# Kernel optimization log

Hardware: AMD Instinct MI355X
Metric: run time of the kernel (lower is better)

## Reference

```python
import jax, jax.numpy as jnp
import numpy as np

B = 256; NROIS = 200; IN = 200; HID = 128; L = 4; H = 8; RATIO = 0.5
K = int(np.ceil(RATIO * NROIS))        # SAGPooling top-k per graph = 100
N = B * NROIS                          # total nodes = 51200
DEG = 32; EPG = NROIS * DEG; E_EDGES = B * EPG  # 1,638,400 edges
EMB = HID * L                          # MHA embed dim = 512
DH = EMB // H

def _xavier(k, shape):
    fan_in, fan_out = shape[-2], shape[-1]
    lim = float(np.sqrt(6.0 / (fan_in + fan_out)))
    return jax.random.uniform(k, shape, jnp.float32, -lim, lim)

def setup_inputs() -> dict:
    key = jax.random.key(0)
    ks = jax.random.split(key, 16)
    x = jax.random.normal(ks[0], (N, IN), jnp.float32)
    # block-diagonal edge list: edges stay within each graph's node range
    src = jax.random.randint(ks[1], (E_EDGES,), 0, NROIS, jnp.int32)
    dst = jax.random.randint(ks[2], (E_EDGES,), 0, NROIS, jnp.int32)
    off = jnp.repeat(jnp.arange(B, dtype=jnp.int32) * NROIS, EPG)
    edge_index = jnp.stack([src + off, dst + off])
    edge_attr = jax.random.normal(ks[3], (E_EDGES,), jnp.float32)  # unused by the math
    batch = jnp.repeat(jnp.arange(B, dtype=jnp.int32), NROIS)
    return dict(
        x=x, edge_index=edge_index, edge_attr=edge_attr, batch=batch,
        gcn_w0=_xavier(ks[4], (IN, HID)),
        gcn_w=_xavier(ks[5], (L - 1, HID, HID)),
        gcn_b=jnp.zeros((L, HID), jnp.float32),
        lin1_w0=_xavier(ks[6], (IN + HID, HID)),
        lin1_w=_xavier(ks[7], (L - 1, 2 * HID, HID)),
        lin1_b=jnp.zeros((L, HID), jnp.float32),
        lin2_w=_xavier(ks[8], (L, HID, HID)),
        lin2_b=jnp.zeros((L, HID), jnp.float32),
        sag_w1=_xavier(ks[9], (HID, 1)),
        sag_w2=_xavier(ks[10], (HID, 1)),
        sag_b=jnp.zeros((1,), jnp.float32),
        mha_in_w=_xavier(ks[11], (3 * EMB, EMB)),
        mha_in_b=jnp.zeros((3 * EMB,), jnp.float32),
        mha_out_w=_xavier(ks[12], (EMB, EMB)),
        mha_out_b=jnp.zeros((EMB,), jnp.float32),
        fin_w=_xavier(ks[13], (EMB, HID)),
        fin_b=jnp.zeros((HID,), jnp.float32),
    )

def _gcn_conv(x, src, dst, W, b):
    xw = x @ W
    deg = jax.ops.segment_sum(jnp.ones_like(dst, jnp.float32), dst, num_segments=N) + 1.0
    dinv = jax.lax.rsqrt(deg)
    norm = dinv[src] * dinv[dst]                     # [E]
    agg = jax.ops.segment_sum(xw[src] * norm[:, None], dst, num_segments=N)
    agg = agg + xw * (dinv * dinv)[:, None]          # self-loop term
    return agg + b

def _gcblock(x, src, dst, gw, gb, l1w, l1b, l2w, l2b):
    x1 = jnp.tanh(_gcn_conv(x, src, dst, gw, gb))
    h = jnp.tanh(jnp.concatenate([x, x1], axis=1) @ l1w + l1b)
    return jnp.tanh(h @ l2w + l2b)

def _sag_pool_pad(z, src, dst, w1, w2, b):
    # SAGPooling score via PyG GraphConv (aggr='add'): lin_rel(sum_j x_j) + lin_root(x_i)
    neigh = jax.ops.segment_sum(z[src], dst, num_segments=N)
    score = (neigh @ w1)[:, 0] + b[0] + (z @ w2)[:, 0]        # [N]
    s3 = score.reshape(B, NROIS)
    vals, idx = jax.lax.top_k(s3, K)                           # [B,K]
    z3 = z.reshape(B, NROIS, HID)
    pooled = jnp.take_along_axis(z3, idx[:, :, None], axis=1) * jnp.tanh(vals)[:, :, None]
    zpad = jnp.zeros_like(z3).at[jnp.arange(B)[:, None], idx].set(pooled)
    return zpad.reshape(N, HID)

def reference(x, edge_index, edge_attr, batch,
              gcn_w0, gcn_w, gcn_b, lin1_w0, lin1_w, lin1_b, lin2_w, lin2_b,
              sag_w1, sag_w2, sag_b,
              mha_in_w, mha_in_b, mha_out_w, mha_out_b, fin_w, fin_b):
    src, dst = edge_index[0], edge_index[1]
    z = x
    pads = []
    for i in range(L):
        gw = gcn_w0 if i == 0 else gcn_w[i - 1]
        l1w = lin1_w0 if i == 0 else lin1_w[i - 1]
        z = _gcblock(z, src, dst, gw, gcn_b[i], l1w, lin1_b[i], lin2_w[i], lin2_b[i])
        pads.append(_sag_pool_pad(z, src, dst, sag_w1, sag_w2, sag_b))
    xc = jnp.concatenate(pads, axis=1).reshape(B, NROIS, EMB)   # [B,S,E]
    # MultiheadAttention (batch_first, eval mode -> no dropout)
    qkv = xc @ mha_in_w.T + mha_in_b                             # [B,S,3E]
    q, k, v = jnp.split(qkv, 3, axis=-1)
    def heads(t):
        return t.reshape(B, NROIS, H, DH).transpose(0, 2, 1, 3)  # [B,H,S,dh]
    q, k, v = heads(q), heads(k), heads(v)
    scores = jnp.einsum('bhqd,bhkd->bhqk', q, k) / np.sqrt(DH)
    attn = jax.nn.softmax(scores, axis=-1)                       # [B,H,S,S]
    o = jnp.einsum('bhqk,bhkd->bhqd', attn, v).transpose(0, 2, 1, 3).reshape(B, NROIS, EMB)
    o = o @ mha_out_w.T + mha_out_b
    attn_weights = attn.mean(axis=1)                             # avg over heads [B,S,S]
    # readout: global_mean_pool over each graph's nrois nodes
    pooled = o.mean(axis=1)                                      # [B,E]
    out = jnp.tanh(pooled @ fin_w + fin_b)                       # [B,HID]
    return out, attn_weights
```

## Files before the change

kernel.cpp:

```cpp
#include <hip/hip_runtime.h>
#include <hip/hip_fp16.h>


#define GB   256
#define SS   200
#define KIN  200
#define HD   128
#define NLAY 4
#define NHD  8
#define TOPK 100
#define NT   (GB * SS)
#define EPG_ 6400
#define NE_  (GB * EPG_)
#define EMB_ 512

typedef _Float16 half8 __attribute__((ext_vector_type(8)));
typedef _Float16 half4v __attribute__((ext_vector_type(4)));
typedef float floatx4 __attribute__((ext_vector_type(4)));

__global__ __launch_bounds__(256) void k_build_A(const int* __restrict__ src,
                                                 const int* __restrict__ dst,
                                                 float* __restrict__ A) {
  int e = blockIdx.x * 256 + threadIdx.x;
  if (e >= NE_) return;
  int d = dst[e], s = src[e];
  int b = d / SS;
  int dl = d - b * SS;
  int sl = s - b * SS;
  atomicAdd(&A[((size_t)b * SS + dl) * SS + sl], 1.0f);
}

__global__ __launch_bounds__(256) void k_dinv(const float* __restrict__ A,
                                              float* __restrict__ dinv) {
  int node = blockIdx.x * 4 + (threadIdx.x >> 6);
  int lane = threadIdx.x & 63;
  const float* r = A + (size_t)node * SS;
  float v = r[lane] + r[lane + 64] + r[lane + 128];
  if (lane < 8) v += r[lane + 192];
#pragma unroll
  for (int o = 32; o; o >>= 1) v += __shfl_xor(v, o);
  if (lane == 0) dinv[node] = rsqrtf(v + 1.0f);
}

__global__ __launch_bounds__(256) void k_prep_all(
    const float* __restrict__ gcn_w0, const float* __restrict__ gcn_w,
    const float* __restrict__ lin1_w0, const float* __restrict__ lin1_w,
    const float* __restrict__ lin2_w,
    __half* __restrict__ whi, __half* __restrict__ wlo) {
  const int mat = blockIdx.x >> 7;
  const int n   = blockIdx.x & 127;
  const int l = mat / 3, which = mat % 3;
  const float* src;
  int K, Kpad;
  if (which == 0) {
    K = l ? HD : KIN;  Kpad = l ? 128 : 256;
    src = l ? gcn_w + (size_t)(l - 1) * HD * HD : gcn_w0;
  } else if (which == 1) {
    K = l ? 2 * HD : KIN + HD;  Kpad = l ? 256 : 384;
    src = l ? lin1_w + (size_t)(l - 1) * 2 * HD * HD : lin1_w0;
  } else {
    K = HD;  Kpad = HD;
    src = lin2_w + (size_t)l * HD * HD;
  }
  int off = (l == 0) ? (which == 0 ? 0 : (which == 1 ? 32768 : 81920))
                     : 98304 + (l - 1) * 65536 +
                       (which == 0 ? 0 : (which == 1 ? 16384 : 49152));
  _Float16* wh = (_Float16*)whi + (size_t)off + (size_t)n * Kpad;
  _Float16* wl = (_Float16*)wlo + (size_t)off + (size_t)n * Kpad;
  for (int k = threadIdx.x; k < Kpad; k += 256) {
    float v = (k < K) ? src[(size_t)k * HD + n] : 0.f;
    _Float16 h = (_Float16)v;
    wh[k] = h;
    wl[k] = (_Float16)(v - (float)h);
  }
}

__global__ __launch_bounds__(256) void k_prep_w16(const float* __restrict__ W,
                                                  __half* __restrict__ W16) {
  int i = blockIdx.x * 256 + threadIdx.x;
  float4 v = reinterpret_cast<const float4*>(W)[i];
  half4v h = {(_Float16)v.x, (_Float16)v.y, (_Float16)v.z, (_Float16)v.w};
  *reinterpret_cast<half4v*>((_Float16*)W16 + (size_t)i * 4) = h;
}

__global__ __launch_bounds__(256) void k_node_mfma(
    const float* __restrict__ in1, int k1,
    const float* __restrict__ in2,
    const __half* __restrict__ Whi, const __half* __restrict__ Wlo,
    int Kpad,
    const float* __restrict__ bias,
    float* __restrict__ out, int doTanh) {
  const int m0 = blockIdx.x * 64;
  const int t = threadIdx.x;
  const int wave = t >> 6, lane = t & 63;
  const int col = lane & 15, quad = lane >> 4;
  const int wm = (wave & 1) * 32;
  const int wn = (wave >> 1) * 64;
  __shared__ __align__(16) _Float16 Ah[64][72];
  __shared__ __align__(16) _Float16 Al[64][72];
  floatx4 acc[2][4] = {};
  const int lr = t >> 2;
  const int lk = (t & 3) * 16;
  const _Float16* Wh = (const _Float16*)Whi;
  const _Float16* Wl = (const _Float16*)Wlo;

  for (int k0 = 0; k0 < Kpad; k0 += 64) {
    __syncthreads();
#pragma unroll
    for (int q = 0; q < 4; ++q) {
      int kg = k0 + lk + q * 4;
      float4 v = {0.f, 0.f, 0.f, 0.f};
      if (kg < k1)
        v = *reinterpret_cast<const float4*>(&in1[(size_t)(m0 + lr) * k1 + kg]);
      else if (in2 && kg < k1 + HD)
        v = *reinterpret_cast<const float4*>(&in2[(size_t)(m0 + lr) * HD + (kg - k1)]);
      half4v h = {(_Float16)v.x, (_Float16)v.y, (_Float16)v.z, (_Float16)v.w};
      half4v lo = {(_Float16)(v.x - (float)h.x), (_Float16)(v.y - (float)h.y),
                   (_Float16)(v.z - (float)h.z), (_Float16)(v.w - (float)h.w)};
      *reinterpret_cast<half4v*>(&Ah[lr][lk + q * 4]) = h;
      *reinterpret_cast<half4v*>(&Al[lr][lk + q * 4]) = lo;
    }
    __syncthreads();
#pragma unroll
    for (int ks = 0; ks < 2; ++ks) {
      half8 ah[2], al[2], bh[4], bl[4];
#pragma unroll
      for (int i = 0; i < 2; ++i) {
        ah[i] = *reinterpret_cast<const half8*>(&Ah[wm + i * 16 + col][ks * 32 + quad * 8]);
        al[i] = *reinterpret_cast<const half8*>(&Al[wm + i * 16 + col][ks * 32 + quad * 8]);
      }
#pragma unroll
      for (int j = 0; j < 4; ++j) {
        const size_t wo = (size_t)(wn + j * 16 + col) * Kpad + k0 + ks * 32 + quad * 8;
        bh[j] = *reinterpret_cast<const half8*>(Wh + wo);
        bl[j] = *reinterpret_cast<const half8*>(Wl + wo);
      }
#pragma unroll
      for (int i = 0; i < 2; ++i)
#pragma unroll
        for (int j = 0; j < 4; ++j) {
          acc[i][j] = __builtin_amdgcn_mfma_f32_16x16x32_f16(ah[i], bh[j], acc[i][j], 0, 0, 0);
          acc[i][j] = __builtin_amdgcn_mfma_f32_16x16x32_f16(ah[i], bl[j], acc[i][j], 0, 0, 0);
          acc[i][j] = __builtin_amdgcn_mfma_f32_16x16x32_f16(al[i], bh[j], acc[i][j], 0, 0, 0);
        }
    }
  }
#pragma unroll
  for (int j = 0; j < 4; ++j) {
    int n = wn + j * 16 + col;
    float bb = bias ? bias[n] : 0.f;
#pragma unroll
    for (int i = 0; i < 2; ++i) {
      int rbase = m0 + wm + i * 16 + quad * 4;
#pragma unroll
      for (int r = 0; r < 4; ++r) {
        float v = acc[i][j][r] + bb;
        if (doTanh) v = tanhf(v);
        out[(size_t)(rbase + r) * HD + n] = v;
      }
    }
  }
}

__global__ __launch_bounds__(256) void k_fused(
    const float* __restrict__ in1, int k1,
    const float* __restrict__ x1,
    const __half* __restrict__ l1wh, const __half* __restrict__ l1wl, int KP1,
    const float* __restrict__ l1b,
    const __half* __restrict__ l2wh, const __half* __restrict__ l2wl,
    const float* __restrict__ l2b,
    const __half* __restrict__ gwh, const __half* __restrict__ gwl,
    float* __restrict__ zout, float* __restrict__ xwout) {
  const int m0 = blockIdx.x * 64;
  const int t = threadIdx.x;
  const int wave = t >> 6, lane = t & 63;
  const int col = lane & 15, quad = lane >> 4;
  const int wm = (wave & 1) * 32;
  const int wn = (wave >> 1) * 64;
  __shared__ __align__(16) _Float16 Ah[64][72];
  __shared__ __align__(16) _Float16 Al[64][72];
  __shared__ __align__(16) _Float16 Hh[64][136];
  __shared__ __align__(16) _Float16 Hl[64][136];
  const int lr = t >> 2;
  const int lk = (t & 3) * 16;

  {
    floatx4 acc[2][4] = {};
    for (int k0 = 0; k0 < KP1; k0 += 64) {
      __syncthreads();
#pragma unroll
      for (int q = 0; q < 4; ++q) {
        int kg = k0 + lk + q * 4;
        float4 v = {0.f, 0.f, 0.f, 0.f};
        if (kg < k1)
          v = *reinterpret_cast<const float4*>(&in1[(size_t)(m0 + lr) * k1 + kg]);
        else if (kg < k1 + HD)
          v = *reinterpret_cast<const float4*>(&x1[(size_t)(m0 + lr) * HD + (kg - k1)]);
        half4v h = {(_Float16)v.x, (_Float16)v.y, (_Float16)v.z, (_Float16)v.w};
        half4v lo = {(_Float16)(v.x - (float)h.x), (_Float16)(v.y - (float)h.y),
                     (_Float16)(v.z - (float)h.z), (_Float16)(v.w - (float)h.w)};
        *reinterpret_cast<half4v*>(&Ah[lr][lk + q * 4]) = h;
        *reinterpret_cast<half4v*>(&Al[lr][lk + q * 4]) = lo;
      }
      __syncthreads();
#pragma unroll
      for (int ks = 0; ks < 2; ++ks) {
        half8 ah[2], al[2], bh[4], bl[4];
#pragma unroll
        for (int i = 0; i < 2; ++i) {
          ah[i] = *reinterpret_cast<const half8*>(&Ah[wm + i * 16 + col][ks * 32 + quad * 8]);
          al[i] = *reinterpret_cast<const half8*>(&Al[wm + i * 16 + col][ks * 32 + quad * 8]);
        }
#pragma unroll
        for (int j = 0; j < 4; ++j) {
          const size_t wo = (size_t)(wn + j * 16 + col) * KP1 + k0 + ks * 32 + quad * 8;
          bh[j] = *reinterpret_cast<const half8*>((const _Float16*)l1wh + wo);
          bl[j] = *reinterpret_cast<const half8*>((const _Float16*)l1wl + wo);
        }
#pragma unroll
        for (int i = 0; i < 2; ++i)
#pragma unroll
          for (int j = 0; j < 4; ++j) {
            acc[i][j] = __builtin_amdgcn_mfma_f32_16x16x32_f16(ah[i], bh[j], acc[i][j], 0, 0, 0);
            acc[i][j] = __builtin_amdgcn_mfma_f32_16x16x32_f16(ah[i], bl[j], acc[i][j], 0, 0, 0);
            acc[i][j] = __builtin_amdgcn_mfma_f32_16x16x32_f16(al[i], bh[j], acc[i][j], 0, 0, 0);
          }
      }
    }
#pragma unroll
    for (int j = 0; j < 4; ++j) {
      int n = wn + j * 16 + col;
      float bb = l1b[n];
#pragma unroll
      for (int i = 0; i < 2; ++i) {
        int rb = wm + i * 16 + quad * 4;
#pragma unroll
        for (int r = 0; r < 4; ++r) {
          float v = tanhf(acc[i][j][r] + bb);
          _Float16 h = (_Float16)v;
          Hh[rb + r][n] = h;
          Hl[rb + r][n] = (_Float16)(v - (float)h);
        }
      }
    }
  }
  __syncthreads();

  {
    floatx4 acc[2][4] = {};
#pragma unroll
    for (int kc = 0; kc < 4; ++kc) {
      half8 ah[2], al[2], bh[4], bl[4];
#pragma unroll
      for (int i = 0; i < 2; ++i) {
        ah[i] = *reinterpret_cast<const half8*>(&Hh[wm + i * 16 + col][kc * 32 + quad * 8]);
        al[i] = *reinterpret_cast<const half8*>(&Hl[wm + i * 16 + col][kc * 32 + quad * 8]);
      }
#pragma unroll
      for (int j = 0; j < 4; ++j) {
        const size_t wo = (size_t)(wn + j * 16 + col) * HD + kc * 32 + quad * 8;
        bh[j] = *reinterpret_cast<const half8*>((const _Float16*)l2wh + wo);
        bl[j] = *reinterpret_cast<const half8*>((const _Float16*)l2wl + wo);
      }
#pragma unroll
      for (int i = 0; i < 2; ++i)
#pragma unroll
        for (int j = 0; j < 4; ++j) {
          acc[i][j] = __builtin_amdgcn_mfma_f32_16x16x32_f16(ah[i], bh[j], acc[i][j], 0, 0, 0);
          acc[i][j] = __builtin_amdgcn_mfma_f32_16x16x32_f16(ah[i], bl[j], acc[i][j], 0, 0, 0);
          acc[i][j] = __builtin_amdgcn_mfma_f32_16x16x32_f16(al[i], bh[j], acc[i][j], 0, 0, 0);
        }
    }
    __syncthreads();
#pragma unroll
    for (int j = 0; j < 4; ++j) {
      int n = wn + j * 16 + col;
      float bb = l2b[n];
#pragma unroll
      for (int i = 0; i < 2; ++i) {
        int rb = wm + i * 16 + quad * 4;
#pragma unroll
        for (int r = 0; r < 4; ++r) {
          float v = tanhf(acc[i][j][r] + bb);
          zout[(size_t)(m0 + rb + r) * HD + n] = v;
          _Float16 h = (_Float16)v;
          Hh[rb + r][n] = h;
          Hl[rb + r][n] = (_Float16)(v - (float)h);
        }
      }
    }
  }
  if (!gwh) return;
  __syncthreads();

  {
    floatx4 acc[2][4] = {};
#pragma unroll
    for (int kc = 0; kc < 4; ++kc) {
      half8 ah[2], al[2], bh[4], bl[4];
#pragma unroll
      for (int i = 0; i < 2; ++i) {
        ah[i] = *reinterpret_cast<const half8*>(&Hh[wm + i * 16 + col][kc * 32 + quad * 8]);
        al[i] = *reinterpret_cast<const half8*>(&Hl[wm + i * 16 + col][kc * 32 + quad * 8]);
      }
#pragma unroll
      for (int j = 0; j < 4; ++j) {
        const size_t wo = (size_t)(wn + j * 16 + col) * HD + kc * 32 + quad * 8;
        bh[j] = *reinterpret_cast<const half8*>((const _Float16*)gwh + wo);
        bl[j] = *reinterpret_cast<const half8*>((const _Float16*)gwl + wo);
      }
#pragma unroll
      for (int i = 0; i < 2; ++i)
#pragma unroll
        for (int j = 0; j < 4; ++j) {
          acc[i][j] = __builtin_amdgcn_mfma_f32_16x16x32_f16(ah[i], bh[j], acc[i][j], 0, 0, 0);
          acc[i][j] = __builtin_amdgcn_mfma_f32_16x16x32_f16(ah[i], bl[j], acc[i][j], 0, 0, 0);
          acc[i][j] = __builtin_amdgcn_mfma_f32_16x16x32_f16(al[i], bh[j], acc[i][j], 0, 0, 0);
        }
    }
#pragma unroll
    for (int j = 0; j < 4; ++j) {
      int n = wn + j * 16 + col;
#pragma unroll
      for (int i = 0; i < 2; ++i) {
        int rb = wm + i * 16 + quad * 4;
#pragma unroll
        for (int r = 0; r < 4; ++r)
          xwout[(size_t)(m0 + rb + r) * HD + n] = acc[i][j][r];
      }
    }
  }
}

__global__ __launch_bounds__(256) void k_agg_mfma(
    const float* __restrict__ A, const float* __restrict__ dinv,
    const float* __restrict__ xw, const float* __restrict__ bias,
    float* __restrict__ out) {
  const int b    = blockIdx.x >> 1;
  const int row0 = (blockIdx.x & 1) * 128;
  const int t = threadIdx.x;
  const int wave = t >> 6, lane = t & 63;
  const int col = lane & 15, quad = lane >> 4;
  const int wm = (wave & 1) * 64, wn = (wave >> 1) * 64;
  __shared__ __align__(16) _Float16 Ah[128][72];
  __shared__ __align__(16) _Float16 Bh[128][72];
  __shared__ __align__(16) _Float16 Bl[128][72];
  __shared__ float dvs[256];
  dvs[t] = (t < SS) ? dinv[b * SS + t] : 0.f;
  floatx4 acc[4][4] = {};
  const float* Ab  = A  + (size_t)b * SS * SS;
  const float* xwb = xw + (size_t)b * SS * HD;
  const int lr = t >> 1, lk = (t & 1) * 32;
  const int d = row0 + lr;
  __syncthreads();

  for (int k0 = 0; k0 < 256; k0 += 64) {
    __syncthreads();
#pragma unroll
    for (int q = 0; q < 8; ++q) {
      int s = k0 + lk + q * 4;
      float4 v = {0.f, 0.f, 0.f, 0.f};
      if (d < SS && s < SS)
        v = *reinterpret_cast<const float4*>(&Ab[(size_t)d * SS + s]);
      if (s + 0 == d) v.x += 1.0f;
      if (s + 1 == d) v.y += 1.0f;
      if (s + 2 == d) v.z += 1.0f;
      if (s + 3 == d) v.w += 1.0f;
      half4v h = {(_Float16)v.x, (_Float16)v.y, (_Float16)v.z, (_Float16)v.w};
      *reinterpret_cast<half4v*>(&Ah[lr][lk + q * 4]) = h;
    }
#pragma unroll
    for (int p = 0; p < 8; ++p) {
      int idx = t + p * 256;
      int c4 = idx & 31, ss = idx >> 5;
      int s = k0 + ss;
      float4 v = {0.f, 0.f, 0.f, 0.f};
      if (s < SS)
        v = *reinterpret_cast<const float4*>(&xwb[(size_t)s * HD + c4 * 4]);
      float dvv = dvs[s & 255];
      int ssx = ss ^ ((c4 & 7) << 3);
      float e[4] = {v.x * dvv, v.y * dvv, v.z * dvv, v.w * dvv};
#pragma unroll
      for (int j = 0; j < 4; ++j) {
        _Float16 h = (_Float16)e[j];
        Bh[c4 * 4 + j][ssx] = h;
        Bl[c4 * 4 + j][ssx] = (_Float16)(e[j] - (float)h);
      }
    }
    __syncthreads();
#pragma unroll
    for (int ks = 0; ks < 2; ++ks) {
      half8 ah[4], bh[4], bl[4];
#pragma unroll
      for (int i = 0; i < 4; ++i)
        ah[i] = *reinterpret_cast<const half8*>(&Ah[wm + i * 16 + col][ks * 32 + quad * 8]);
#pragma unroll
      for (int j = 0; j < 4; ++j) {
        int n = wn + j * 16 + col;
        int koff = (ks * 32 + quad * 8) ^ (((n >> 2) & 7) << 3);
        bh[j] = *reinterpret_cast<const half8*>(&Bh[n][koff]);
        bl[j] = *reinterpret_cast<const half8*>(&Bl[n][koff]);
      }
#pragma unroll
      for (int i = 0; i < 4; ++i)
#pragma unroll
        for (int j = 0; j < 4; ++j) {
          acc[i][j] = __builtin_amdgcn_mfma_f32_16x16x32_f16(ah[i], bh[j], acc[i][j], 0, 0, 0);
          acc[i][j] = __builtin_amdgcn_mfma_f32_16x16x32_f16(ah[i], bl[j], acc[i][j], 0, 0, 0);
        }
    }
  }
#pragma unroll
  for (int j = 0; j < 4; ++j) {
    int n = wn + j * 16 + col;
    float bb = bias[n];
#pragma unroll
    for (int i = 0; i < 4; ++i) {
      int rbase = row0 + wm + i * 16 + quad * 4;
#pragma unroll
      for (int r = 0; r < 4; ++r) {
        int row = rbase + r;
        if (row < SS)
          out[((size_t)b * SS + row) * HD + n] = tanhf(dvs[row] * acc[i][j][r] + bb);
      }
    }
  }
}

__global__ __launch_bounds__(256) void k_sag(
    const float* __restrict__ z, const float* __restrict__ A,
    const float* __restrict__ w1, const float* __restrict__ w2,
    const float* __restrict__ sb,
    __half* __restrict__ xch, __half* __restrict__ xcl, int layer) {
  const int b = blockIdx.x, t = threadIdx.x;
  __shared__ float w1s[HD], w2s[HD];
  __shared__ float zw1[SS], sc[SS], fac[SS];
  if (t < HD) { w1s[t] = w1[t]; w2s[t] = w2[t]; }
  __syncthreads();
  float a2 = 0.f;
  if (t < SS) {
    const float4* zr = reinterpret_cast<const float4*>(&z[((size_t)b * SS + t) * HD]);
    float a1 = 0.f;
#pragma unroll
    for (int q = 0; q < HD / 4; ++q) {
      float4 v = zr[q];
      a1 += v.x * w1s[4 * q] + v.y * w1s[4 * q + 1] + v.z * w1s[4 * q + 2] + v.w * w1s[4 * q + 3];
      a2 += v.x * w2s[4 * q] + v.y * w2s[4 * q + 1] + v.z * w2s[4 * q + 2] + v.w * w2s[4 * q + 3];
    }
    zw1[t] = a1;
  }
  __syncthreads();
  if (t < SS) {
    float s0 = 0.f, s1 = 0.f, s2 = 0.f, s3 = 0.f;
    const float4* ar = reinterpret_cast<const float4*>(&A[((size_t)b * SS + t) * SS]);
#pragma unroll
    for (int q = 0; q < SS / 4; q += 4) {
      float4 v0 = ar[q], v1 = ar[q + 1];
      float4 v2 = (q + 2 < SS / 4) ? ar[q + 2] : float4{0.f, 0.f, 0.f, 0.f};
      float4 v3 = (q + 3 < SS / 4) ? ar[q + 3] : float4{0.f, 0.f, 0.f, 0.f};
      s0 += v0.x * zw1[4 * q] + v0.y * zw1[4 * q + 1] + v0.z * zw1[4 * q + 2] + v0.w * zw1[4 * q + 3];
      s1 += v1.x * zw1[4 * q + 4] + v1.y * zw1[4 * q + 5] + v1.z * zw1[4 * q + 6] + v1.w * zw1[4 * q + 7];
      if (q + 2 < SS / 4)
        s2 += v2.x * zw1[4 * q + 8] + v2.y * zw1[4 * q + 9] + v2.z * zw1[4 * q + 10] + v2.w * zw1[4 * q + 11];
      if (q + 3 < SS / 4)
        s3 += v3.x * zw1[4 * q + 12] + v3.y * zw1[4 * q + 13] + v3.z * zw1[4 * q + 14] + v3.w * zw1[4 * q + 15];
    }
    sc[t] = sb[0] + a2 + ((s0 + s1) + (s2 + s3));
  }
  __syncthreads();
  if (t < SS) {
    float si = sc[t];
    int cnt = 0;
    for (int j = 0; j < SS; ++j) {
      float sj = sc[j];
      cnt += (sj > si || (sj == si && j < t)) ? 1 : 0;
    }
    fac[t] = (cnt < TOPK) ? tanhf(si) : 0.f;
  }
  __syncthreads();
  _Float16* xh = (_Float16*)xch;
  _Float16* xl = (_Float16*)xcl;
  for (int idx = t; idx < SS * HD; idx += 256) {
    int row = idx >> 7, c = idx & 127;
    float v = fac[row] * z[((size_t)b * SS + row) * HD + c];
    _Float16 h = (_Float16)v;
    size_t o = ((size_t)b * SS + row) * EMB_ + layer * HD + c;
    xh[o] = h;
    xl[o] = (_Float16)(v - (float)h);
  }
}

__global__ __launch_bounds__(256) void k_proj(
    const __half* __restrict__ xch, const __half* __restrict__ Win16,
    const float* __restrict__ bin, __half* __restrict__ QKh) {
  const int wg = (blockIdx.x & 7) * 400 + (blockIdx.x >> 3);
  const int bm = wg >> 3;
  const int bn = wg & 7;
  const int m0 = bm * 128, n0 = bn * 128;
  const int t = threadIdx.x;
  const int wave = t >> 6, lane = t & 63;
  const int col = lane & 15, quad = lane >> 4;
  const int wm = (wave & 1) * 64;
  const int wn = (wave >> 1) * 64;
  __shared__ __align__(16) _Float16 As[128][64];
  __shared__ __align__(16) _Float16 Bs[128][64];
  floatx4 acc[4][4] = {};
  const _Float16* X = (const _Float16*)xch;
  const _Float16* W = (const _Float16*)Win16;

  const int srow = lane >> 3;
  const int sch  = (lane & 7) ^ srow;
  const int arow = wave * 8 + srow;
  const int fsw = col & 7;

  for (int k0 = 0; k0 < EMB_; k0 += 64) {
#pragma unroll
    for (int q = 0; q < 4; ++q) {
      const _Float16* ga = X + (size_t)(m0 + q * 32 + arow) * EMB_ + k0 + sch * 8;
      __builtin_amdgcn_global_load_lds(
          (const __attribute__((address_space(1))) void*)ga,
          (__attribute__((address_space(3))) void*)((char*)&As[0][0] + q * 4096 + wave * 1024),
          16, 0, 0);
      const _Float16* gb = W + (size_t)(n0 + q * 32 + arow) * EMB_ + k0 + sch * 8;
      __builtin_amdgcn_global_load_lds(
          (const __attribute__((address_space(1))) void*)gb,
          (__attribute__((address_space(3))) void*)((char*)&Bs[0][0] + q * 4096 + wave * 1024),
          16, 0, 0);
    }
    __syncthreads();
#pragma unroll
    for (int ks = 0; ks < 2; ++ks) {
      const int ch = (ks * 4 + quad) ^ fsw;
      half8 af[4], bf[4];
#pragma unroll
      for (int i = 0; i < 4; ++i)
        af[i] = *reinterpret_cast<const half8*>(
            (const char*)&As[0][0] + (wm + i * 16 + col) * 128 + ch * 16);
#pragma unroll
      for (int j = 0; j < 4; ++j)
        bf[j] = *reinterpret_cast<const half8*>(
            (const char*)&Bs[0][0] + (wn + j * 16 + col) * 128 + ch * 16);
#pragma unroll
      for (int i = 0; i < 4; ++i)
#pragma unroll
        for (int j = 0; j < 4; ++j)
          acc[i][j] = __builtin_amdgcn_mfma_f32_16x16x32_f16(af[i], bf[j], acc[i][j], 0, 0, 0);
    }
    __syncthreads();
  }
#pragma unroll
  for (int j = 0; j < 4; ++j) {
    int c = n0 + wn + j * 16 + col;
    float bb = bin[c];
#pragma unroll
    for (int i = 0; i < 4; ++i) {
      int rbase = m0 + wm + i * 16 + quad * 4;
#pragma unroll
      for (int r = 0; r < 4; ++r)
        QKh[(size_t)(rbase + r) * 1024 + c] = __float2half(acc[i][j][r] + bb);
    }
  }
}

__global__ __launch_bounds__(256) void k_attn(
    const __half* __restrict__ QKh,
    float* __restrict__ cpbuf,
    float* __restrict__ attn) {
  const int bx = (blockIdx.x & 7) * 416 + (blockIdx.x >> 3);
  const int b  = bx / 13;
  const int it = bx % 13;
  const int i0 = it * 16;
  const int rows = (SS - i0 >= 16) ? 16 : (SS - i0);
  const int t    = threadIdx.x;
  const int wave = t >> 6;
  const int lane = t & 63;
  const int col  = lane & 15;
  const int quad = lane >> 4;
  const int srow_ = t >> 4;
  const int ssub_ = t & 15;

  __shared__ __align__(16) float Ss[16][212];

  float am[13];
  int   soff[13];
  int   kmax = 0;
#pragma unroll
  for (int k = 0; k < 13; ++k) {
    int idx = t + (k << 8);
    am[k] = 0.f;
    if (idx < rows * 200) {
      int i = idx / 200;
      soff[k] = idx + 12 * i;
      kmax = k + 1;
    } else soff[k] = 0;
  }

  const _Float16* Qbase = (const _Float16*)QKh + (size_t)b * SS * 1024;
  const _Float16* qrow = Qbase + (size_t)(i0 + col) * 1024 + quad * 8;
  const _Float16* krow[4];
#pragma unroll
  for (int m = 0; m < 4; ++m) {
    int jt = wave + m * 4;
    krow[m] = Qbase + (size_t)(jt * 16 + col) * 1024 + 512 + quad * 8;
  }

  for (int h = 0; h < NHD; ++h) {
    const int hoff = h * 64;
    half8 a0 = *reinterpret_cast<const half8*>(qrow + hoff);
    half8 a1 = *reinterpret_cast<const half8*>(qrow + hoff + 32);
#pragma unroll
    for (int m = 0; m < 4; ++m) {
      int jt = wave + m * 4;
      if (jt < 13) {
        half8 b0 = *reinterpret_cast<const half8*>(krow[m] + hoff);
        half8 b1 = *reinterpret_cast<const half8*>(krow[m] + hoff + 32);
        floatx4 acc = {0.f, 0.f, 0.f, 0.f};
        acc = __builtin_amdgcn_mfma_f32_16x16x32_f16(a0, b0, acc, 0, 0, 0);
        acc = __builtin_amdgcn_mfma_f32_16x16x32_f16(a1, b1, acc, 0, 0, 0);
#pragma unroll
        for (int r = 0; r < 4; ++r)
          Ss[quad * 4 + r][jt * 16 + col] = acc[r] * 0.125f;
      }
    }
    __syncthreads();
    if (srow_ < rows) {
      float v[13];
      float mx = -1e30f;
#pragma unroll
      for (int i2 = 0; i2 < 13; ++i2) {
        int c = ssub_ + i2 * 16;
        v[i2] = (c < 200) ? Ss[srow_][c] : -1e30f;
        mx = fmaxf(mx, v[i2]);
      }
#pragma unroll
      for (int m = 8; m; m >>= 1) mx = fmaxf(mx, __shfl_xor(mx, m));
      float sum = 0.f;
#pragma unroll
      for (int i2 = 0; i2 < 13; ++i2) {
        v[i2] = __expf(v[i2] - mx);
        sum += v[i2];
      }
#pragma unroll
      for (int m = 8; m; m >>= 1) sum += __shfl_xor(sum, m);
      float rl = 1.0f / sum;
#pragma unroll
      for (int i2 = 0; i2 < 13; ++i2) {
        int c = ssub_ + i2 * 16;
        if (c < 200) Ss[srow_][c] = v[i2] * rl;
      }
    }
    __syncthreads();
    const float* sflat = &Ss[0][0];
#pragma unroll
    for (int k = 0; k < 13; ++k)
      if (k < kmax) am[k] += sflat[soff[k]] * 0.125f;
    if (t < SS) {
      float s = 0.f;
      for (int i = 0; i < rows; ++i) s += Ss[i][t];
      atomicAdd(&cpbuf[((size_t)b * NHD + h) * SS + t], s);
    }
    __syncthreads();
  }
  float* abase = &attn[((size_t)b * SS + i0) * SS];
#pragma unroll
  for (int k = 0; k < 13; ++k)
    if (k < kmax) abase[t + (k << 8)] = am[k];
}

__global__ __launch_bounds__(256) void k_pool(
    const __half* __restrict__ xch, const __half* __restrict__ xcl,
    const float* __restrict__ cpbuf,
    const float* __restrict__ Win, const float* __restrict__ bin,
    float* __restrict__ pooled) {
  const int b = blockIdx.x, t = threadIdx.x;
  __shared__ float cps[NHD][SS];
  __shared__ float tvs[NHD][EMB_];
  for (int idx = t; idx < NHD * SS; idx += 256) {
    int h = idx / SS, j = idx - h * SS;
    cps[h][j] = cpbuf[((size_t)b * NHD + h) * SS + j];
  }
  __syncthreads();
  const _Float16* xh = (const _Float16*)xch + (size_t)b * SS * EMB_;
  const _Float16* xl = (const _Float16*)xcl + (size_t)b * SS * EMB_;
  float a0[NHD] = {0.f}, a1[NHD] = {0.f};
  for (int j = 0; j < SS; ++j) {
    float x0 = (float)xh[(size_t)j * EMB_ + t] + (float)xl[(size_t)j * EMB_ + t];
    float x1 = (float)xh[(size_t)j * EMB_ + t + 256] + (float)xl[(size_t)j * EMB_ + t + 256];
#pragma unroll
    for (int h = 0; h < NHD; ++h) {
      float c = cps[h][j];
      a0[h] += c * x0; a1[h] += c * x1;
    }
  }
#pragma unroll
  for (int h = 0; h < NHD; ++h) { tvs[h][t] = a0[h]; tvs[h][t + 256] = a1[h]; }
  __syncthreads();
  const int wv = t >> 6, lane = t & 63;
  for (int e = wv; e < EMB_; e += 4) {
    int h = e >> 6;
    const float* wr = Win + (size_t)(2 * EMB_ + e) * EMB_;
    float s = 0.f;
#pragma unroll
    for (int q = 0; q < 8; ++q) s += wr[lane + q * 64] * tvs[h][lane + q * 64];
#pragma unroll
    for (int o = 32; o; o >>= 1) s += __shfl_xor(s, o);
    if (lane == 0) pooled[(size_t)b * EMB_ + e] = bin[2 * EMB_ + e] * (float)SS + s;
  }
}

__global__ __launch_bounds__(256) void k_final(
    const float* __restrict__ pooled, const float* __restrict__ Wout,
    const float* __restrict__ bout, const float* __restrict__ finw,
    const float* __restrict__ finb, float* __restrict__ out) {
  const int b = blockIdx.x, t = threadIdx.x;
  __shared__ float pl[EMB_], po[EMB_];
  for (int k = t; k < EMB_; k += 256) pl[k] = pooled[(size_t)b * EMB_ + k] * (1.0f / (float)SS);
  __syncthreads();
  for (int e = t; e < EMB_; e += 256) {
    const float* wr = &Wout[(size_t)e * EMB_];
    float a = bout[e];
    for (int k = 0; k < EMB_; ++k) a += wr[k] * pl[k];
    po[e] = a;
  }
  __syncthreads();
  if (t < HD) {
    float a = finb[t];
    for (int e = 0; e < EMB_; ++e) a += po[e] * finw[(size_t)e * HD + t];
    out[(size_t)b * HD + t] = tanhf(a);
  }
}

extern "C" void kernel_launch(void* const* d_in, const int* in_sizes, int n_in,
                              void* d_out, int out_size, void* d_ws, size_t ws_size,
                              hipStream_t stream) {
  const float* x         = (const float*)d_in[0];
  const int*   ei        = (const int*)d_in[1];
  const float* gcn_w0    = (const float*)d_in[4];
  const float* gcn_w     = (const float*)d_in[5];
  const float* gcn_b     = (const float*)d_in[6];
  const float* lin1_w0   = (const float*)d_in[7];
  const float* lin1_w    = (const float*)d_in[8];
  const float* lin1_b    = (const float*)d_in[9];
  const float* lin2_w    = (const float*)d_in[10];
  const float* lin2_b    = (const float*)d_in[11];
  const float* sag_w1    = (const float*)d_in[12];
  const float* sag_w2    = (const float*)d_in[13];
  const float* sag_b     = (const float*)d_in[14];
  const float* mha_in_w  = (const float*)d_in[15];
  const float* mha_in_b  = (const float*)d_in[16];
  const float* mha_out_w = (const float*)d_in[17];
  const float* mha_out_b = (const float*)d_in[18];
  const float* fin_w     = (const float*)d_in[19];
  const float* fin_b     = (const float*)d_in[20];

  float* ws     = (float*)d_ws;
  float* dinv   = ws;
  float* Araw   = dinv + NT;
  float* buf0   = Araw + (size_t)GB * SS * SS;
  float* buf1   = buf0 + (size_t)NT * HD;
  float* zbuf   = buf1 + (size_t)NT * HD;
  float* xcf    = zbuf + (size_t)NT * HD;
  __half* xch   = (__half*)xcf;
  __half* xcl   = xch + (size_t)NT * EMB_;
  float* pooled = xcf + (size_t)NT * EMB_;
  __half* QKh  = (__half*)Araw;
  float* cpbuf = Araw + 26214400;

  float* outp = (float*)d_out;
  float* attn = outp + (size_t)GB * HD;

  __half* whi   = (__half*)attn;
  __half* wlo   = whi + 294912;
  __half* Win16 = wlo + 294912;

  hipMemsetAsync(Araw, 0, (size_t)GB * SS * SS * sizeof(float), stream);

  k_prep_all<<<12 * 128, 256, 0, stream>>>(gcn_w0, gcn_w, lin1_w0, lin1_w, lin2_w, whi, wlo);
  k_prep_w16<<<512, 256, 0, stream>>>(mha_in_w, Win16);
  k_build_A<<<NE_ / 256, 256, 0, stream>>>(ei, ei + NE_, Araw);
  k_dinv<<<NT / 4, 256, 0, stream>>>(Araw, dinv);

  static const int KP1[4]  = {384, 256, 256, 256};
  static const int OFFg[4] = {0, 98304, 163840, 229376};
  static const int OFF1[4] = {32768, 114688, 180224, 245760};
  static const int OFF2[4] = {81920, 147456, 212992, 278528};

  k_node_mfma<<<NT / 64, 256, 0, stream>>>(x, KIN, nullptr,
                                           whi + OFFg[0], wlo + OFFg[0], 256,
                                           nullptr, buf0, 0);

  for (int l = 0; l < NLAY; ++l) {
    const float* zin = (l == 0) ? x : zbuf;
    int k1 = (l == 0) ? KIN : HD;
    k_agg_mfma<<<GB * 2, 256, 0, stream>>>(Araw, dinv, buf0, gcn_b + l * HD, buf1);
    k_fused<<<NT / 64, 256, 0, stream>>>(
        zin, k1, buf1,
        whi + OFF1[l], wlo + OFF1[l], KP1[l], lin1_b + l * HD,
        whi + OFF2[l], wlo + OFF2[l], lin2_b + l * HD,
        (l < NLAY - 1) ? whi + OFFg[l + 1] : (const __half*)nullptr,
        (l < NLAY - 1) ? wlo + OFFg[l + 1] : (const __half*)nullptr,
        zbuf, buf0);
    k_sag<<<GB, 256, 0, stream>>>(zbuf, Araw, sag_w1, sag_w2, sag_b, xch, xcl, l);
  }

  hipMemsetAsync(cpbuf, 0, (size_t)GB * NHD * SS * sizeof(float), stream);
  k_proj<<<(NT / 128) * 8, 256, 0, stream>>>(xch, Win16, mha_in_b, QKh);
  k_attn<<<GB * 13, 256, 0, stream>>>(QKh, cpbuf, attn);
  k_pool<<<GB, 256, 0, stream>>>(xch, xcl, cpbuf, mha_in_w, mha_in_b, pooled);
  k_final<<<GB, 256, 0, stream>>>(pooled, mha_out_w, mha_out_b, fin_w, fin_b, outp);
}
```

Before: 1.411 ms.

## Convert adjacency to fp16 once and stream it into LDS via direct global loads

Adds a one-time pass that converts the dense per-graph adjacency matrix to fp16 (with padding). The aggregation kernel then loads A tiles straight into LDS with global_load_lds using an XOR swizzle, and moves the self-loop term into the epilogue as dinv^2 * xw. The SAG scoring kernel also reads the fp16 adjacency. This halves A traffic across the four layers and drops per-element conversion work, at the cost of an extra conversion kernel, extra workspace, and relying on edge counts being exactly representable in fp16.

```diff
diff --git a/kernel.cpp b/kernel.cpp
--- a/kernel.cpp
+++ b/kernel.cpp
@@ -13,6 +13,8 @@
 #define EPG_ 6400
 #define NE_  (GB * EPG_)
 #define EMB_ 512
+#define NA_  (GB * SS * SS)
+#define NA_PAD (NA_ + 16384)
 
 typedef _Float16 half8 __attribute__((ext_vector_type(8)));
 typedef _Float16 half4v __attribute__((ext_vector_type(4)));
@@ -40,6 +42,18 @@
 #pragma unroll
   for (int o = 32; o; o >>= 1) v += __shfl_xor(v, o);
   if (lane == 0) dinv[node] = rsqrtf(v + 1.0f);
+}
+
+__global__ __launch_bounds__(256) void k_prep_a16(const float* __restrict__ A,
+                                                  __half* __restrict__ A16) {
+  size_t i4 = ((size_t)blockIdx.x * 256 + threadIdx.x) * 4;
+  if (i4 >= NA_PAD) return;
+  half4v h = {(_Float16)0.f, (_Float16)0.f, (_Float16)0.f, (_Float16)0.f};
+  if (i4 < NA_) {
+    float4 v = *reinterpret_cast<const float4*>(A + i4);
+    h = {(_Float16)v.x, (_Float16)v.y, (_Float16)v.z, (_Float16)v.w};
+  }
+  *reinterpret_cast<half4v*>((_Float16*)A16 + i4) = h;
 }
 
 __global__ __launch_bounds__(256) void k_prep_all(
@@ -333,7 +347,7 @@
 }
 
 __global__ __launch_bounds__(256) void k_agg_mfma(
-    const float* __restrict__ A, const float* __restrict__ dinv,
+    const __half* __restrict__ A16, const float* __restrict__ dinv,
     const float* __restrict__ xw, const float* __restrict__ bias,
     float* __restrict__ out) {
   const int b    = blockIdx.x >> 1;
@@ -342,32 +356,29 @@
   const int wave = t >> 6, lane = t & 63;
   const int col = lane & 15, quad = lane >> 4;
   const int wm = (wave & 1) * 64, wn = (wave >> 1) * 64;
-  __shared__ __align__(16) _Float16 Ah[128][72];
+  __shared__ __align__(16) _Float16 As[128][64];
   __shared__ __align__(16) _Float16 Bh[128][72];
   __shared__ __align__(16) _Float16 Bl[128][72];
   __shared__ float dvs[256];
   dvs[t] = (t < SS) ? dinv[b * SS + t] : 0.f;
   floatx4 acc[4][4] = {};
-  const float* Ab  = A  + (size_t)b * SS * SS;
+  const _Float16* Ab = (const _Float16*)A16 + (size_t)b * SS * SS;
   const float* xwb = xw + (size_t)b * SS * HD;
-  const int lr = t >> 1, lk = (t & 1) * 32;
-  const int d = row0 + lr;
+  const int srow = lane >> 3;
+  const int sch  = (lane & 7) ^ srow;
+  const int arow = wave * 8 + srow;
+  const int fsw  = col & 7;
   __syncthreads();
 
   for (int k0 = 0; k0 < 256; k0 += 64) {
     __syncthreads();
 #pragma unroll
-    for (int q = 0; q < 8; ++q) {
-      int s = k0 + lk + q * 4;
-      float4 v = {0.f, 0.f, 0.f, 0.f};
-      if (d < SS && s < SS)
-        v = *reinterpret_cast<const float4*>(&Ab[(size_t)d * SS + s]);
-      if (s + 0 == d) v.x += 1.0f;
-      if (s + 1 == d) v.y += 1.0f;
-      if (s + 2 == d) v.z += 1.0f;
-      if (s + 3 == d) v.w += 1.0f;
-      half4v h = {(_Float16)v.x, (_Float16)v.y, (_Float16)v.z, (_Float16)v.w};
-      *reinterpret_cast<half4v*>(&Ah[lr][lk + q * 4]) = h;
+    for (int q = 0; q < 4; ++q) {
+      const _Float16* ga = Ab + (size_t)(row0 + q * 32 + arow) * SS + k0 + sch * 8;
+      __builtin_amdgcn_global_load_lds(
+          (const __attribute__((address_space(1))) void*)ga,
+          (__attribute__((address_space(3))) void*)((char*)&As[0][0] + q * 4096 + wave * 1024),
+          16, 0, 0);
     }
 #pragma unroll
     for (int p = 0; p < 8; ++p) {
@@ -390,10 +401,12 @@
     __syncthreads();
 #pragma unroll
     for (int ks = 0; ks < 2; ++ks) {
+      const int ch = (ks * 4 + quad) ^ fsw;
       half8 ah[4], bh[4], bl[4];
 #pragma unroll
       for (int i = 0; i < 4; ++i)
-        ah[i] = *reinterpret_cast<const half8*>(&Ah[wm + i * 16 + col][ks * 32 + quad * 8]);
+        ah[i] = *reinterpret_cast<const half8*>(
+            (const char*)&As[0][0] + (wm + i * 16 + col) * 128 + ch * 16);
 #pragma unroll
       for (int j = 0; j < 4; ++j) {
         int n = wn + j * 16 + col;
@@ -420,15 +433,19 @@
 #pragma unroll
       for (int r = 0; r < 4; ++r) {
         int row = rbase + r;
-        if (row < SS)
-          out[((size_t)b * SS + row) * HD + n] = tanhf(dvs[row] * acc[i][j][r] + bb);
+        if (row < SS) {
+          float dv = dvs[row];
+          float xwv = xwb[(size_t)row * HD + n];
+          out[((size_t)b * SS + row) * HD + n] =
+              tanhf(dv * acc[i][j][r] + dv * dv * xwv + bb);
+        }
       }
     }
   }
 }
 
 __global__ __launch_bounds__(256) void k_sag(
-    const float* __restrict__ z, const float* __restrict__ A,
+    const float* __restrict__ z, const __half* __restrict__ A16,
     const float* __restrict__ w1, const float* __restrict__ w2,
     const float* __restrict__ sb,
     __half* __restrict__ xch, __half* __restrict__ xcl, int layer) {
@@ -451,21 +468,24 @@
   }
   __syncthreads();
   if (t < SS) {
-    float s0 = 0.f, s1 = 0.f, s2 = 0.f, s3 = 0.f;
-    const float4* ar = reinterpret_cast<const float4*>(&A[((size_t)b * SS + t) * SS]);
-#pragma unroll
-    for (int q = 0; q < SS / 4; q += 4) {
-      float4 v0 = ar[q], v1 = ar[q + 1];
-      float4 v2 = (q + 2 < SS / 4) ? ar[q + 2] : float4{0.f, 0.f, 0.f, 0.f};
-      float4 v3 = (q + 3 < SS / 4) ? ar[q + 3] : float4{0.f, 0.f, 0.f, 0.f};
-      s0 += v0.x * zw1[4 * q] + v0.y * zw1[4 * q + 1] + v0.z * zw1[4 * q + 2] + v0.w * zw1[4 * q + 3];
-      s1 += v1.x * zw1[4 * q + 4] + v1.y * zw1[4 * q + 5] + v1.z * zw1[4 * q + 6] + v1.w * zw1[4 * q + 7];
-      if (q + 2 < SS / 4)
-        s2 += v2.x * zw1[4 * q + 8] + v2.y * zw1[4 * q + 9] + v2.z * zw1[4 * q + 10] + v2.w * zw1[4 * q + 11];
-      if (q + 3 < SS / 4)
-        s3 += v3.x * zw1[4 * q + 12] + v3.y * zw1[4 * q + 13] + v3.z * zw1[4 * q + 14] + v3.w * zw1[4 * q + 15];
-    }
-    sc[t] = sb[0] + a2 + ((s0 + s1) + (s2 + s3));
+    float s0 = 0.f, s1 = 0.f;
+    const half8* ar = reinterpret_cast<const half8*>(
+        (const _Float16*)A16 + (size_t)(b * SS + t) * SS);
+#pragma unroll 4
+    for (int q = 0; q < 24; q += 2) {
+      half8 v0 = ar[q], v1 = ar[q + 1];
+#pragma unroll
+      for (int e = 0; e < 8; ++e) {
+        s0 += (float)v0[e] * zw1[8 * q + e];
+        s1 += (float)v1[e] * zw1[8 * q + 8 + e];
+      }
+    }
+    {
+      half8 v0 = ar[24];
+#pragma unroll
+      for (int e = 0; e < 8; ++e) s0 += (float)v0[e] * zw1[192 + e];
+    }
+    sc[t] = sb[0] + a2 + s0 + s1;
   }
   __syncthreads();
   if (t < SS) {
@@ -772,6 +792,7 @@
   __half* whi   = (__half*)attn;
   __half* wlo   = whi + 294912;
   __half* Win16 = wlo + 294912;
+  __half* A16   = Win16 + 524288;
 
   hipMemsetAsync(Araw, 0, (size_t)GB * SS * SS * sizeof(float), stream);
 
@@ -779,6 +800,7 @@
   k_prep_w16<<<512, 256, 0, stream>>>(mha_in_w, Win16);
   k_build_A<<<NE_ / 256, 256, 0, stream>>>(ei, ei + NE_, Araw);
   k_dinv<<<NT / 4, 256, 0, stream>>>(Araw, dinv);
+  k_prep_a16<<<NA_PAD / 1024, 256, 0, stream>>>(Araw, A16);
 
   static const int KP1[4]  = {384, 256, 256, 256};
   static const int OFFg[4] = {0, 98304, 163840, 229376};
@@ -792,7 +814,7 @@
   for (int l = 0; l < NLAY; ++l) {
     const float* zin = (l == 0) ? x : zbuf;
     int k1 = (l == 0) ? KIN : HD;
-    k_agg_mfma<<<GB * 2, 256, 0, stream>>>(Araw, dinv, buf0, gcn_b + l * HD, buf1);
+    k_agg_mfma<<<GB * 2, 256, 0, stream>>>(A16, dinv, buf0, gcn_b + l * HD, buf1);
     k_fused<<<NT / 64, 256, 0, stream>>>(
         zin, k1, buf1,
         whi + OFF1[l], wlo + OFF1[l], KP1[l], lin1_b + l * HD,
@@ -800,7 +822,7 @@
         (l < NLAY - 1) ? whi + OFFg[l + 1] : (const __half*)nullptr,
         (l < NLAY - 1) ? wlo + OFFg[l + 1] : (const __half*)nullptr,
         zbuf, buf0);
-    k_sag<<<GB, 256, 0, stream>>>(zbuf, Araw, sag_w1, sag_w2, sag_b, xch, xcl, l);
+    k_sag<<<GB, 256, 0, stream>>>(zbuf, A16, sag_w1, sag_w2, sag_b, xch, xcl, l);
   }
 
   hipMemsetAsync(cpbuf, 0, (size_t)GB * NHD * SS * sizeof(float), stream);
```

Measured after the change: 1.413 ms. About the same (+0.2%).
